# Kernel tuning notes

Hardware: AMD Instinct MI355X
Metric: run time of the kernel (lower is better)

Reference implementation:

```python
import jax, jax.numpy as jnp
import numpy as np

KNN_K = 8
WINDOW = 3  # temporal_window + 1 candidate frames
LN_EPS = 1e-5
NORM_EPS = 1e-12


def setup_inputs() -> dict:
    key = jax.random.key(0)
    B, T, M, D, H = 2, 8, 512, 1024, 1024
    ks = jax.random.split(key, 12)
    s = 0.02
    return {
        "z": jax.random.normal(ks[0], (B, T, M, D), jnp.float32),
        "Wq": jax.random.normal(ks[1], (D, D), jnp.float32) * s,
        "Wv": jax.random.normal(ks[2], (D, D), jnp.float32) * s,
        "Wout": jax.random.normal(ks[3], (D, D), jnp.float32) * s,
        "ln_w": jnp.ones((D,), jnp.float32),
        "ln_b": jnp.zeros((D,), jnp.float32),
        "Watt_q": jax.random.normal(ks[4], (D, D), jnp.float32) * s,
        "Watt_k": jax.random.normal(ks[5], (D, D), jnp.float32) * s,
        "W_ih": jax.random.normal(ks[6], (3 * H, D), jnp.float32) * s,
        "W_hh": jax.random.normal(ks[7], (3 * H, H), jnp.float32) * s,
        "b_ih": jnp.zeros((3 * H,), jnp.float32),
        "b_hh": jnp.zeros((3 * H,), jnp.float32),
        "W_mf": jax.random.normal(ks[8], (D, H), jnp.float32) * s,
        "b_mf": jnp.zeros((D,), jnp.float32),
    }


def _forward(z, Wq, Wv, Wout, ln_w, ln_b, Watt_q, Watt_k,
             W_ih, W_hh, b_ih, b_hh, W_mf, b_mf):
    B, T, M, D = z.shape
    H = W_hh.shape[1]
    # cosine normalization (torch F.normalize with eps clamp)
    zn = z / jnp.maximum(jnp.linalg.norm(z, axis=-1, keepdims=True), NORM_EPS)
    mem = jnp.zeros((B, M, H), z.dtype)
    b_ar = jnp.arange(B)[:, None, None]
    outs = []
    for t in range(T):  # T is static; fully vectorized over B, M, k inside
        tts = t - jnp.arange(WINDOW)          # candidate frames t, t-1, t-2
        valid = tts >= 0                      # [W]
        cand = zn[:, jnp.clip(tts, 0)]        # [B,W,M,D]
        # cosine similarity query nodes at t vs all candidates (dt-major order)
        sim = jnp.einsum('bmd,bwnd->bmwn', zn[:, t], cand).reshape(B, M, WINDOW * M)
        sim = jnp.where(jnp.repeat(valid, M)[None, None, :], sim, -jnp.inf)
        vals, idx = jax.lax.top_k(sim, KNN_K)  # [B,M,k]
        dt = idx // M
        j = idx % M
        tt = jnp.clip(t - dt, 0)
        Kfeat = z[b_ar, tt, j]                 # [B,M,k,D] gathered neighbors
        # GAT quirk faithful to source: scalar logit scale from node 0's query,
        # first output coordinate only, shared across all nodes of (b,t)
        s0 = z[:, t, 0] @ Watt_q[0]            # [B]
        kh_sum = (Kfeat @ Watt_k.T).sum(-1)    # [B,M,k]
        att = jax.nn.softmax(s0[:, None, None] * kh_sum, axis=-1)
        alpha = 0.5 * vals + 0.5 * att         # [B,M,k]
        msg = jnp.einsum('bmk,bmkd->bmd', alpha, Kfeat @ Wv.T)
        h_t = z[:, t]                          # [B,M,D]
        x = msg + h_t @ Wq.T
        mu = x.mean(-1, keepdims=True)
        var = ((x - mu) ** 2).mean(-1, keepdims=True)
        x = (x - mu) / jnp.sqrt(var + LN_EPS) * ln_w + ln_b
        inp = x @ Wout.T
        # torch GRUCell: gates ordered (r, z, n)
        gi = inp @ W_ih.T + b_ih               # [B,M,3H]
        gh = mem @ W_hh.T + b_hh
        ir, iz, inn = jnp.split(gi, 3, axis=-1)
        hr, hz, hn = jnp.split(gh, 3, axis=-1)
        r = jax.nn.sigmoid(ir + hr)
        zg = jax.nn.sigmoid(iz + hz)
        n = jnp.tanh(inn + r * hn)
        mem = (1.0 - zg) * n + zg * mem
        outs.append(h_t + mem @ W_mf.T + b_mf)
    h = jnp.stack(outs, axis=1)                # [B,T,M,D]
    return h, mem


def reference(z, Wq, Wv, Wout, ln_w, ln_b, Watt_q, Watt_k,
              W_ih, W_hh, b_ih, b_hh, W_mf, b_mf):
    return _forward(z, Wq, Wv, Wout, ln_w, ln_b, Watt_q, Watt_k,
                    W_ih, W_hh, b_ih, b_hh, W_mf, b_mf)
```

## Files before the change

### kernel.cpp

```cpp
#include <hip/hip_runtime.h>
#include <hip/hip_bf16.h>
#include <math.h>

#define B_ 2
#define T_ 8
#define M_ 512
#define D_ 1024
#define H_ 1024
#define NC_ 1536
#define KNN 8

typedef __hip_bfloat16 bf16;
typedef short v8s __attribute__((ext_vector_type(8)));
typedef float v4f __attribute__((ext_vector_type(4)));

__device__ __forceinline__ float b2f(short s) {
  union { unsigned u; float f; } x; x.u = ((unsigned)(unsigned short)s) << 16; return x.f;
}

__device__ __forceinline__ void async16(const void* g, void* l) {
  __builtin_amdgcn_global_load_lds(
      (const __attribute__((address_space(1))) void*)g,
      (__attribute__((address_space(3))) void*)l, 16, 0, 0);
}

__device__ __forceinline__ void mfma_loop(const bf16* __restrict__ A,
                                          const bf16* __restrict__ Bp,
                                          int K, v4f (&acc)[4][4],
                                          bf16* sA, bf16* sB)
{
  const int tid  = threadIdx.x;
  const int lane = tid & 63;
  const int wave = tid >> 6;
  const int quad = lane >> 4;
  const int l15  = lane & 15;
  const int wr = (wave >> 1) * 64;
  const int wc = (wave & 1) * 64;

  const int r0 = tid >> 2, g0 = (tid & 3) ^ ((r0 >> 1) & 3);
  const int c1 = tid + 256;
  const int r1 = c1 >> 2,  g1 = (c1 & 3) ^ ((r1 >> 1) & 3);

  const bf16* a0p = A  + (size_t)r0*K + g0*8;
  const bf16* a1p = A  + (size_t)r1*K + g1*8;
  const bf16* b0p = Bp + (size_t)r0*K + g0*8;
  const bf16* b1p = Bp + (size_t)r1*K + g1*8;
  bf16* la0 = sA + tid*8;  bf16* la1 = sA + c1*8;
  bf16* lb0 = sB + tid*8;  bf16* lb1 = sB + c1*8;

  int aoff[4], boff[4];
  #pragma unroll
  for (int i = 0; i < 4; ++i) {
    int ra = wr + i*16 + l15;
    aoff[i] = (ra*4 + (quad ^ ((ra >> 1) & 3))) * 8;
    int rb = wc + i*16 + l15;
    boff[i] = (rb*4 + (quad ^ ((rb >> 1) & 3))) * 8;
  }

  for (int k0 = 0; k0 < K; k0 += 32) {
    __syncthreads();
    async16(a0p + k0, la0);
    async16(a1p + k0, la1);
    async16(b0p + k0, lb0);
    async16(b1p + k0, lb1);
    __syncthreads();
    v8s af[4], bfr[4];
    #pragma unroll
    for (int i = 0; i < 4; ++i) af[i]  = *(const v8s*)(sA + aoff[i]);
    #pragma unroll
    for (int i = 0; i < 4; ++i) bfr[i] = *(const v8s*)(sB + boff[i]);
    #pragma unroll
    for (int mi = 0; mi < 4; ++mi)
      #pragma unroll
      for (int ni = 0; ni < 4; ++ni)
        acc[mi][ni] = __builtin_amdgcn_mfma_f32_16x16x32_bf16(
            af[mi], bfr[ni], acc[mi][ni], 0, 0, 0);
  }
}

template<bool DUAL, bool HASBIAS, bool HASADD, bool OUTBF>
__global__ __launch_bounds__(256) void k_bgemm(
    const bf16* __restrict__ A1, const bf16* __restrict__ B1,
    const bf16* __restrict__ A2, const bf16* __restrict__ B2,
    const float* __restrict__ bias, const float* __restrict__ add,
    void* __restrict__ Cv, int N, int K)
{
  __shared__ bf16 sA[128*32];
  __shared__ bf16 sB[128*32];
  v4f acc[4][4];
  #pragma unroll
  for (int i = 0; i < 4; ++i)
    #pragma unroll
    for (int j = 0; j < 4; ++j) acc[i][j] = (v4f){0.f,0.f,0.f,0.f};

  const int row0 = blockIdx.y * 128, col0 = blockIdx.x * 128;
  mfma_loop(A1 + (size_t)row0*K, B1 + (size_t)col0*K, K, acc, sA, sB);
  if constexpr (DUAL)
    mfma_loop(A2 + (size_t)row0*K, B2 + (size_t)col0*K, K, acc, sA, sB);

  const int tid = threadIdx.x, lane = tid & 63, wave = tid >> 6;
  const int quad = lane >> 4, l15 = lane & 15;
  const int wr = (wave >> 1) * 64, wc = (wave & 1) * 64;

  #pragma unroll
  for (int ni = 0; ni < 4; ++ni) {
    const int col = col0 + wc + ni*16 + l15;
    float bv = 0.f;
    if constexpr (HASBIAS) bv = bias[col];
    #pragma unroll
    for (int mi = 0; mi < 4; ++mi) {
      const int rowb = row0 + wr + mi*16 + quad*4;
      #pragma unroll
      for (int reg = 0; reg < 4; ++reg) {
        const int row = rowb + reg;
        float v = acc[mi][ni][reg] + bv;
        if constexpr (HASADD) v += add[(size_t)row*N + col];
        if constexpr (OUTBF)
          ((bf16*)Cv)[(size_t)row*N + col] = __float2bfloat16(v);
        else
          ((float*)Cv)[(size_t)row*N + col] = v;
      }
    }
  }
}

__global__ __launch_bounds__(256) void k_sims(const bf16* __restrict__ znhi,
                                              const bf16* __restrict__ znlo,
                                              float* __restrict__ sim)
{
  __shared__ bf16 sAh[128*32];
  __shared__ bf16 sAl[128*32];
  __shared__ bf16 sBh[128*32];
  __shared__ bf16 sBl[128*32];

  const int zi = blockIdx.z;
  const int w  = zi % 3;
  const int bt = zi / 3;
  const int b  = bt / T_;
  const int t  = bt % T_;
  if (w > t) return;
  const int tw = t - w;
  const int arow0 = bt*M_ + blockIdx.y*128;
  const int brow0 = (b*T_ + tw)*M_ + blockIdx.x*128;

  const bf16* Ah = znhi + (size_t)arow0*D_;
  const bf16* Al = znlo + (size_t)arow0*D_;
  const bf16* Bh = znhi + (size_t)brow0*D_;
  const bf16* Bl = znlo + (size_t)brow0*D_;

  v4f acc[4][4];
  #pragma unroll
  for (int i = 0; i < 4; ++i)
    #pragma unroll
    for (int j = 0; j < 4; ++j) acc[i][j] = (v4f){0.f,0.f,0.f,0.f};

  const int tid  = threadIdx.x;
  const int lane = tid & 63;
  const int wave = tid >> 6;
  const int quad = lane >> 4;
  const int l15  = lane & 15;
  const int wr = (wave >> 1) * 64;
  const int wc = (wave & 1) * 64;

  const int r0 = tid >> 2, g0 = (tid & 3) ^ ((r0 >> 1) & 3);
  const int c1 = tid + 256;
  const int r1 = c1 >> 2,  g1 = (c1 & 3) ^ ((r1 >> 1) & 3);
  const size_t o0 = (size_t)r0*D_ + g0*8;
  const size_t o1 = (size_t)r1*D_ + g1*8;

  int aoff[4], boff[4];
  #pragma unroll
  for (int i = 0; i < 4; ++i) {
    int ra = wr + i*16 + l15;
    aoff[i] = (ra*4 + (quad ^ ((ra >> 1) & 3))) * 8;
    int rb = wc + i*16 + l15;
    boff[i] = (rb*4 + (quad ^ ((rb >> 1) & 3))) * 8;
  }

  for (int k0 = 0; k0 < D_; k0 += 32) {
    __syncthreads();
    async16(Ah + o0 + k0, sAh + tid*8);
    async16(Ah + o1 + k0, sAh + c1*8);
    async16(Al + o0 + k0, sAl + tid*8);
    async16(Al + o1 + k0, sAl + c1*8);
    async16(Bh + o0 + k0, sBh + tid*8);
    async16(Bh + o1 + k0, sBh + c1*8);
    async16(Bl + o0 + k0, sBl + tid*8);
    async16(Bl + o1 + k0, sBl + c1*8);
    __syncthreads();
    v8s ah[4], al[4], bh[4], bl[4];
    #pragma unroll
    for (int i = 0; i < 4; ++i) {
      ah[i] = *(const v8s*)(sAh + aoff[i]);
      al[i] = *(const v8s*)(sAl + aoff[i]);
      bh[i] = *(const v8s*)(sBh + boff[i]);
      bl[i] = *(const v8s*)(sBl + boff[i]);
    }
    #pragma unroll
    for (int mi = 0; mi < 4; ++mi)
      #pragma unroll
      for (int ni = 0; ni < 4; ++ni) {
        acc[mi][ni] = __builtin_amdgcn_mfma_f32_16x16x32_bf16(ah[mi], bh[ni], acc[mi][ni], 0, 0, 0);
        acc[mi][ni] = __builtin_amdgcn_mfma_f32_16x16x32_bf16(ah[mi], bl[ni], acc[mi][ni], 0, 0, 0);
        acc[mi][ni] = __builtin_amdgcn_mfma_f32_16x16x32_bf16(al[mi], bh[ni], acc[mi][ni], 0, 0, 0);
      }
  }

  float* C = sim + (size_t)bt*M_*NC_;
  const int rowbase = blockIdx.y*128 + wr;
  const int colbase = w*M_ + blockIdx.x*128 + wc;
  #pragma unroll
  for (int ni = 0; ni < 4; ++ni) {
    const int col = colbase + ni*16 + l15;
    #pragma unroll
    for (int mi = 0; mi < 4; ++mi) {
      const int rowb = rowbase + mi*16 + quad*4;
      #pragma unroll
      for (int reg = 0; reg < 4; ++reg)
        C[(size_t)(rowb+reg)*NC_ + col] = acc[mi][ni][reg];
    }
  }
}


__global__ __launch_bounds__(256) void k_cast(const float* __restrict__ src,
                                              bf16* __restrict__ dst, int n4) {
  int i = blockIdx.x*256 + threadIdx.x;
  if (i < n4) {
    float4 v = ((const float4*)src)[i];
    bf16* p = dst + (size_t)i*4;
    p[0] = __float2bfloat16(v.x); p[1] = __float2bfloat16(v.y);
    p[2] = __float2bfloat16(v.z); p[3] = __float2bfloat16(v.w);
  }
}

__global__ __launch_bounds__(256) void k_colsum(const float* __restrict__ Wk,
                                                float* __restrict__ wk_sum) {
  int d = blockIdx.x*256 + threadIdx.x;
  float s = 0.f;
  for (int i = 0; i < D_; ++i) s += Wk[(size_t)i*D_ + d];
  wk_sum[d] = s;
}

__global__ __launch_bounds__(64) void k_s0(const float* __restrict__ z,
                                           const float* __restrict__ Wattq,
                                           float* __restrict__ s0) {
  int bt = blockIdx.x;
  const float* zr = z + (size_t)bt*M_*D_;
  float p = 0.f;
  for (int d = threadIdx.x; d < D_; d += 64) p += zr[d]*Wattq[d];
  for (int o = 32; o; o >>= 1) p += __shfl_down(p, o, 64);
  if (threadIdx.x == 0) s0[bt] = p;
}

__global__ __launch_bounds__(256) void k_kh(const float* __restrict__ z,
                                            const float* __restrict__ wks,
                                            float* __restrict__ kh) {
  int wave = threadIdx.x >> 6, l = threadIdx.x & 63;
  int r = blockIdx.x*4 + wave;
  const float* zp = z + (size_t)r*D_ + l*16;
  const float* wp = wks + l*16;
  float p = 0.f;
  #pragma unroll
  for (int j = 0; j < 4; ++j) {
    float4 a = *(const float4*)(zp + j*4);
    float4 b = *(const float4*)(wp + j*4);
    p += a.x*b.x + a.y*b.y + a.z*b.z + a.w*b.w;
  }
  for (int o = 32; o; o >>= 1) p += __shfl_down(p, o, 64);
  if (l == 0) kh[r] = p;
}

__global__ __launch_bounds__(256) void k_znsplit(const float* __restrict__ z,
                                                 bf16* __restrict__ znhi,
                                                 bf16* __restrict__ znlo) {
  int row = blockIdx.x, tid = threadIdx.x;
  const float* zr = z + (size_t)row*D_;
  int d = tid*4;
  float4 v = *(const float4*)(zr + d);
  float ss = v.x*v.x + v.y*v.y + v.z*v.z + v.w*v.w;
  for (int o=32;o;o>>=1) ss += __shfl_down(ss,o,64);
  __shared__ float ps[4];
  if ((tid&63)==0) ps[tid>>6] = ss;
  __syncthreads();
  float s = ps[0]+ps[1]+ps[2]+ps[3];
  float rn = 1.0f / fmaxf(sqrtf(s), 1e-12f);
  float zn[4] = {v.x*rn, v.y*rn, v.z*rn, v.w*rn};
  bf16 hi[4], lo[4];
  #pragma unroll
  for (int j = 0; j < 4; ++j) {
    hi[j] = __float2bfloat16(zn[j]);
    lo[j] = __float2bfloat16(zn[j] - b2f(*(short*)&hi[j]));
  }
  *(short4*)(znhi + (size_t)row*D_ + d) = *(short4*)hi;
  *(short4*)(znlo + (size_t)row*D_ + d) = *(short4*)lo;
}

__global__ __launch_bounds__(256) void k_topk(
    const float* __restrict__ sim, const float* __restrict__ kh,
    const float* __restrict__ s0, const bf16* __restrict__ zb,
    bf16* __restrict__ kbarb)
{
  const int wave = threadIdx.x >> 6, l = threadIdx.x & 63;
  const int r  = blockIdx.x*4 + wave;
  const int bt = r >> 9, m = r & 511;
  const int b  = bt >> 3, t = bt & 7;
  const float* srow = sim + (size_t)bt*M_*NC_ + (size_t)m*NC_;
  const int limit = (t >= 2) ? NC_ : ((t == 1) ? 2*M_ : M_);

  float v[24];
  #pragma unroll
  for (int j = 0; j < 24; ++j) {
    int i = j*64 + l;
    v[j] = (i < limit) ? srow[i] : -INFINITY;
  }

  float selv[KNN]; int seli[KNN];
  #pragma unroll
  for (int k = 0; k < KNN; ++k) {
    float bv = v[0]; int bj = 0;
    #pragma unroll
    for (int j = 1; j < 24; ++j)
      if (v[j] > bv) { bv = v[j]; bj = j; }
    int bi = bj*64 + l;
    #pragma unroll
    for (int o = 1; o < 64; o <<= 1) {
      float ov = __shfl_xor(bv, o, 64);
      int   oi = __shfl_xor(bi, o, 64);
      if (ov > bv || (ov == bv && oi < bi)) { bv = ov; bi = oi; }
    }
    selv[k] = bv; seli[k] = bi;
    if ((bi & 63) == l) {
      int jj = bi >> 6;
      #pragma unroll
      for (int j = 0; j < 24; ++j) if (j == jj) v[j] = -INFINITY;
    }
  }

  float khv = 0.f;
  if (l < KNN) {
    int idx = seli[l];
    int w = idx >> 9, n = idx & 511;
    int tt = t - w;
    khv = kh[(b*T_ + tt)*M_ + n];
  }
  float s0v = s0[bt];
  float att[KNN], mx = -INFINITY;
  #pragma unroll
  for (int k = 0; k < KNN; ++k) { att[k] = s0v * __shfl(khv, k, 64); mx = fmaxf(mx, att[k]); }
  float den = 0.f;
  #pragma unroll
  for (int k = 0; k < KNN; ++k) { att[k] = expf(att[k]-mx); den += att[k]; }
  float rden = 1.0f/den;
  float alpha[KNN];
  #pragma unroll
  for (int k = 0; k < KNN; ++k) alpha[k] = 0.5f*selv[k] + 0.5f*att[k]*rden;

  const int d0 = l*16;
  float o[16];
  #pragma unroll
  for (int e = 0; e < 16; ++e) o[e] = 0.f;
  #pragma unroll
  for (int k = 0; k < KNN; ++k) {
    int idx = seli[k];
    int w = idx >> 9, n = idx & 511;
    int tt = t - w;
    const bf16* zp = zb + ((size_t)((b*T_ + tt)*M_ + n))*D_ + d0;
    v8s z0 = *(const v8s*)zp;
    v8s z1 = *(const v8s*)(zp + 8);
    float al = alpha[k];
    #pragma unroll
    for (int e = 0; e < 8; ++e) {
      o[e]   = fmaf(al, b2f(z0[e]), o[e]);
      o[8+e] = fmaf(al, b2f(z1[e]), o[8+e]);
    }
  }
  bf16* kp = kbarb + (size_t)r*D_ + d0;
  short outv[16];
  #pragma unroll
  for (int e = 0; e < 16; ++e) { bf16 h = __float2bfloat16(o[e]); outv[e] = *(short*)&h; }
  *(v8s*)kp       = *(v8s*)outv;
  *(v8s*)(kp + 8) = *(v8s*)(outv + 8);
}

__global__ __launch_bounds__(256) void k_ln(const float* __restrict__ X,
                                            const float* __restrict__ lw,
                                            const float* __restrict__ lb,
                                            bf16* __restrict__ Xb) {
  int r = blockIdx.x, tid = threadIdx.x;
  const float* xp = X + (size_t)r*D_;
  int d = tid*4;
  float4 v = *(const float4*)(xp + d);
  float s  = v.x+v.y+v.z+v.w;
  float ss = v.x*v.x+v.y*v.y+v.z*v.z+v.w*v.w;
  for (int o=32;o;o>>=1){ s += __shfl_down(s,o,64); ss += __shfl_down(ss,o,64); }
  __shared__ float rs[4], rss[4];
  if ((tid&63)==0){ rs[tid>>6]=s; rss[tid>>6]=ss; }
  __syncthreads();
  float mu  = (rs[0]+rs[1]+rs[2]+rs[3]) * (1.f/D_);
  float var = (rss[0]+rss[1]+rss[2]+rss[3]) * (1.f/D_) - mu*mu;
  float rstd = rsqrtf(var + 1e-5f);
  float4 w  = *(const float4*)(lw+d);
  float4 bb = *(const float4*)(lb+d);
  bf16* op = Xb + (size_t)r*D_ + d;
  op[0] = __float2bfloat16((v.x-mu)*rstd*w.x + bb.x);
  op[1] = __float2bfloat16((v.y-mu)*rstd*w.y + bb.y);
  op[2] = __float2bfloat16((v.z-mu)*rstd*w.z + bb.z);
  op[3] = __float2bfloat16((v.w-mu)*rstd*w.w + bb.w);
}

__global__ __launch_bounds__(256) void k_gru(
    const float* __restrict__ gi, const float* __restrict__ gh,
    float* __restrict__ mem, bf16* __restrict__ memb,
    bf16* __restrict__ memhb, int t)
{
  int gid = blockIdx.x*256 + threadIdx.x;
  int row = gid >> 10, h = gid & 1023;
  int b = row >> 9, m = row & 511;
  size_t girow = ((size_t)((b*T_ + t)*M_ + m))*(3*H_);
  float ir  = gi[girow + h];
  float iz  = gi[girow + H_ + h];
  float in_ = gi[girow + 2*H_ + h];
  size_t ghrow = (size_t)row*(3*H_);
  float hr = gh[ghrow + h];
  float hz = gh[ghrow + H_ + h];
  float hn = gh[ghrow + 2*H_ + h];
  float rg = 1.f/(1.f+expf(-(ir+hr)));
  float zg = 1.f/(1.f+expf(-(iz+hz)));
  float n  = tanhf(in_ + rg*hn);
  float mold = mem[gid];
  float mnew = (1.f-zg)*n + zg*mold;
  mem[gid] = mnew;
  memb[gid] = __float2bfloat16(mnew);
  memhb[((size_t)((b*T_ + t)*M_ + m))*H_ + h] = __float2bfloat16(mnew);
}

extern "C" void kernel_launch(void* const* d_in, const int* in_sizes, int n_in,
                              void* d_out, int out_size, void* d_ws, size_t ws_size,
                              hipStream_t stream) {
  (void)in_sizes; (void)n_in; (void)out_size; (void)ws_size;
  const float* z      = (const float*)d_in[0];
  const float* Wq     = (const float*)d_in[1];
  const float* Wv     = (const float*)d_in[2];
  const float* Wout   = (const float*)d_in[3];
  const float* ln_w   = (const float*)d_in[4];
  const float* ln_b   = (const float*)d_in[5];
  const float* Watt_q = (const float*)d_in[6];
  const float* Watt_k = (const float*)d_in[7];
  const float* W_ih   = (const float*)d_in[8];
  const float* W_hh   = (const float*)d_in[9];
  const float* b_ih   = (const float*)d_in[10];
  const float* b_hh   = (const float*)d_in[11];
  const float* W_mf   = (const float*)d_in[12];
  const float* b_mf   = (const float*)d_in[13];
  float* out = (float*)d_out;
  float* ws  = (float*)d_ws;

  float* GI    = ws;
  float* sim   = ws;
  float* X     = ws;
  float* gs    = ws + 25165824;
  float* mem   = ws + 28311552;
  bf16*  Xb    = (bf16*)(ws + 29360128);
  bf16*  znhi  = Xb;
  bf16*  zb    = (bf16*)(ws + 33554432);
  bf16*  kbarb = (bf16*)(ws + 37748736);
  bf16*  INPb  = kbarb;
  bf16*  memb  = (bf16*)(ws + 41943040);
  bf16*  memhb = (bf16*)(ws + 42467328);
  bf16*  znlo  = memhb;
  bf16*  Wqb   = (bf16*)(ws + 46661632);
  bf16*  Wvb   = Wqb + 1048576;
  bf16*  Woutb = Wqb + 2097152;
  bf16*  Wihb  = Wqb + 3145728;
  bf16*  Whhb  = Wqb + 6291456;
  bf16*  Wmfb  = Wqb + 9437184;
  float* wks   = ws + 51904512;
  float* s0    = ws + 51905536;
  float* kh    = ws + 51905552;

  k_cast<<<dim3(1024), dim3(256), 0, stream>>>(Wq,   Wqb,   262144);
  k_cast<<<dim3(1024), dim3(256), 0, stream>>>(Wv,   Wvb,   262144);
  k_cast<<<dim3(1024), dim3(256), 0, stream>>>(Wout, Woutb, 262144);
  k_cast<<<dim3(3072), dim3(256), 0, stream>>>(W_ih, Wihb,  786432);
  k_cast<<<dim3(3072), dim3(256), 0, stream>>>(W_hh, Whhb,  786432);
  k_cast<<<dim3(1024), dim3(256), 0, stream>>>(W_mf, Wmfb,  262144);
  k_cast<<<dim3(8192), dim3(256), 0, stream>>>(z,    zb,   2097152);

  k_colsum <<<dim3(4),    dim3(256), 0, stream>>>(Watt_k, wks);
  k_s0     <<<dim3(16),   dim3(64),  0, stream>>>(z, Watt_q, s0);
  k_kh     <<<dim3(2048), dim3(256), 0, stream>>>(z, wks, kh);
  k_znsplit<<<dim3(8192), dim3(256), 0, stream>>>(z, znhi, znlo);

  k_sims<<<dim3(4,4,48), dim3(256), 0, stream>>>(znhi, znlo, sim);

  k_topk<<<dim3(2048), dim3(256), 0, stream>>>(sim, kh, s0, zb, kbarb);

  k_bgemm<true,false,false,false><<<dim3(8,64), dim3(256), 0, stream>>>(
      kbarb, Wvb, zb, Wqb, nullptr, nullptr, X, D_, D_);

  k_ln<<<dim3(8192), dim3(256), 0, stream>>>(X, ln_w, ln_b, Xb);

  k_bgemm<false,false,false,true><<<dim3(8,64), dim3(256), 0, stream>>>(
      Xb, Woutb, nullptr, nullptr, nullptr, nullptr, INPb, D_, D_);

  k_bgemm<false,true,false,false><<<dim3(24,64), dim3(256), 0, stream>>>(
      INPb, Wihb, nullptr, nullptr, b_ih, nullptr, GI, 3*H_, D_);

  hipMemsetAsync(mem,  0, (size_t)1048576*sizeof(float), stream);
  hipMemsetAsync(memb, 0, (size_t)1048576*sizeof(bf16),  stream);

  for (int t = 0; t < T_; ++t) {
    k_bgemm<false,true,false,false><<<dim3(24,8), dim3(256), 0, stream>>>(
        memb, Whhb, nullptr, nullptr, b_hh, nullptr, gs, 3*H_, H_);
    k_gru<<<dim3(4096), dim3(256), 0, stream>>>(GI, gs, mem, memb, memhb, t);
  }

  k_bgemm<false,true,true,false><<<dim3(8,64), dim3(256), 0, stream>>>(
      memhb, Wmfb, nullptr, nullptr, b_mf, z, out, D_, H_);

  hipMemcpyAsync(out + (size_t)B_*T_*M_*D_, mem, (size_t)1048576*sizeof(float),
                 hipMemcpyDeviceToDevice, stream);
}
```

Before: 827.0 us.

## Fuse GRU gate GEMM with cell update, merge prep kernels, store bf16 intermediates

Replaces the per-step W_hh GEMM plus separate GRU elementwise kernel with one fused kernel that computes all three gate tiles in registers and applies the GRU update in the epilogue. The hidden-state bf16 buffer is ping-ponged between steps to avoid read/write races. The six weight casts become one launch, the z cast, norm split and kh dot product are merged into one pass over z, and the X and GI intermediates are stored as bf16 instead of fp32. Together these cut launches and memory traffic, but the bf16 X and GI add rounding error, and the fused GRU grid is small (128 blocks) with no k-loop pipelining.

New measurement: 858.7 us. 1.04x slower.

```diff
diff --git a/kernel.cpp b/kernel.cpp
--- a/kernel.cpp
+++ b/kernel.cpp
@@ -16,6 +16,9 @@
 
 __device__ __forceinline__ float b2f(short s) {
   union { unsigned u; float f; } x; x.u = ((unsigned)(unsigned short)s) << 16; return x.f;
+}
+__device__ __forceinline__ short f2b(float f) {
+  bf16 h = __float2bfloat16(f); return *(short*)&h;
 }
 
 __device__ __forceinline__ void async16(const void* g, void* l) {
@@ -222,16 +225,135 @@
   }
 }
 
-
-__global__ __launch_bounds__(256) void k_cast(const float* __restrict__ src,
-                                              bf16* __restrict__ dst, int n4) {
+__global__ __launch_bounds__(256) void k_fgru(
+    const bf16* __restrict__ membIn, const bf16* __restrict__ Whhb,
+    const bf16* __restrict__ gib, const float* __restrict__ b_hh,
+    float* __restrict__ mem, bf16* __restrict__ membOut,
+    bf16* __restrict__ memhb, int t)
+{
+  __shared__ bf16 sA[128*32];
+  __shared__ bf16 sB[3][64*32];
+
+  const int row0 = blockIdx.y * 128;
+  const int col0 = blockIdx.x * 64;
+
+  v4f acc[3][4][2];
+  #pragma unroll
+  for (int g = 0; g < 3; ++g)
+    #pragma unroll
+    for (int i = 0; i < 4; ++i)
+      #pragma unroll
+      for (int j = 0; j < 2; ++j) acc[g][i][j] = (v4f){0.f,0.f,0.f,0.f};
+
+  const int tid  = threadIdx.x;
+  const int lane = tid & 63;
+  const int wave = tid >> 6;
+  const int quad = lane >> 4;
+  const int l15  = lane & 15;
+  const int wr = (wave >> 1) * 64;
+  const int wc = (wave & 1) * 32;
+
+  const int rA0 = tid >> 2, gA0 = (tid & 3) ^ ((rA0 >> 1) & 3);
+  const int c1 = tid + 256;
+  const int rA1 = c1 >> 2,  gA1 = (c1 & 3) ^ ((rA1 >> 1) & 3);
+  const int rB = tid >> 2,  gB  = (tid & 3) ^ ((rB >> 1) & 3);
+
+  const bf16* Ap = membIn + (size_t)row0*H_;
+  const size_t aofs0 = (size_t)rA0*H_ + gA0*8;
+  const size_t aofs1 = (size_t)rA1*H_ + gA1*8;
+  const size_t bofs  = (size_t)(col0 + rB)*H_ + gB*8;
+
+  int aoff[4], boff[2];
+  #pragma unroll
+  for (int i = 0; i < 4; ++i) {
+    int ra = wr + i*16 + l15;
+    aoff[i] = (ra*4 + (quad ^ ((ra >> 1) & 3))) * 8;
+  }
+  #pragma unroll
+  for (int i = 0; i < 2; ++i) {
+    int rb = wc + i*16 + l15;
+    boff[i] = (rb*4 + (quad ^ ((rb >> 1) & 3))) * 8;
+  }
+
+  for (int k0 = 0; k0 < H_; k0 += 32) {
+    __syncthreads();
+    async16(Ap + aofs0 + k0, sA + tid*8);
+    async16(Ap + aofs1 + k0, sA + c1*8);
+    async16(Whhb + bofs + k0,           sB[0] + tid*8);
+    async16(Whhb + 1048576 + bofs + k0, sB[1] + tid*8);
+    async16(Whhb + 2097152 + bofs + k0, sB[2] + tid*8);
+    __syncthreads();
+    v8s af[4], bfr[3][2];
+    #pragma unroll
+    for (int i = 0; i < 4; ++i) af[i] = *(const v8s*)(sA + aoff[i]);
+    #pragma unroll
+    for (int g = 0; g < 3; ++g)
+      #pragma unroll
+      for (int i = 0; i < 2; ++i) bfr[g][i] = *(const v8s*)(sB[g] + boff[i]);
+    #pragma unroll
+    for (int g = 0; g < 3; ++g)
+      #pragma unroll
+      for (int mi = 0; mi < 4; ++mi)
+        #pragma unroll
+        for (int ni = 0; ni < 2; ++ni)
+          acc[g][mi][ni] = __builtin_amdgcn_mfma_f32_16x16x32_bf16(
+              af[mi], bfr[g][ni], acc[g][mi][ni], 0, 0, 0);
+  }
+
+  #pragma unroll
+  for (int ni = 0; ni < 2; ++ni) {
+    const int col = col0 + wc + ni*16 + l15;
+    const float bhr = b_hh[col];
+    const float bhz = b_hh[H_ + col];
+    const float bhn = b_hh[2*H_ + col];
+    #pragma unroll
+    for (int mi = 0; mi < 4; ++mi) {
+      const int rowb = row0 + wr + mi*16 + quad*4;
+      #pragma unroll
+      for (int reg = 0; reg < 4; ++reg) {
+        const int row = rowb + reg;
+        const int b = row >> 9, m = row & 511;
+        const size_t btm = (size_t)((b*T_ + t)*M_ + m);
+        const bf16* gp = gib + btm*(3*H_);
+        float ir  = b2f(*(const short*)(gp + col));
+        float iz  = b2f(*(const short*)(gp + H_ + col));
+        float inn = b2f(*(const short*)(gp + 2*H_ + col));
+        float hr = acc[0][mi][ni][reg] + bhr;
+        float hz = acc[1][mi][ni][reg] + bhz;
+        float hn = acc[2][mi][ni][reg] + bhn;
+        float rg = 1.f/(1.f + expf(-(ir + hr)));
+        float zg = 1.f/(1.f + expf(-(iz + hz)));
+        float n  = tanhf(inn + rg*hn);
+        const size_t mo = (size_t)row*H_ + col;
+        float mold = mem[mo];
+        float mnew = (1.f - zg)*n + zg*mold;
+        mem[mo] = mnew;
+        bf16 mb = __float2bfloat16(mnew);
+        membOut[mo] = mb;
+        memhb[btm*H_ + col] = mb;
+      }
+    }
+  }
+}
+
+
+__global__ __launch_bounds__(256) void k_castall(
+    const float* __restrict__ w0, const float* __restrict__ w1,
+    const float* __restrict__ w2, const float* __restrict__ w3,
+    const float* __restrict__ w4, const float* __restrict__ w5,
+    bf16* __restrict__ dst)
+{
   int i = blockIdx.x*256 + threadIdx.x;
-  if (i < n4) {
-    float4 v = ((const float4*)src)[i];
-    bf16* p = dst + (size_t)i*4;
-    p[0] = __float2bfloat16(v.x); p[1] = __float2bfloat16(v.y);
-    p[2] = __float2bfloat16(v.z); p[3] = __float2bfloat16(v.w);
-  }
+  const float* src; int base;
+  if      (i <  262144) { src = w0; base = 0; }
+  else if (i <  524288) { src = w1; base = 262144; }
+  else if (i <  786432) { src = w2; base = 524288; }
+  else if (i < 1572864) { src = w3; base = 786432; }
+  else if (i < 2359296) { src = w4; base = 1572864; }
+  else                  { src = w5; base = 2359296; }
+  float4 v = ((const float4*)src)[i - base];
+  short4 o = make_short4(f2b(v.x), f2b(v.y), f2b(v.z), f2b(v.w));
+  *(short4*)(dst + (size_t)i*4) = o;
 }
 
 __global__ __launch_bounds__(256) void k_colsum(const float* __restrict__ Wk,
@@ -253,31 +375,17 @@
   if (threadIdx.x == 0) s0[bt] = p;
 }
 
-__global__ __launch_bounds__(256) void k_kh(const float* __restrict__ z,
-                                            const float* __restrict__ wks,
-                                            float* __restrict__ kh) {
-  int wave = threadIdx.x >> 6, l = threadIdx.x & 63;
-  int r = blockIdx.x*4 + wave;
-  const float* zp = z + (size_t)r*D_ + l*16;
-  const float* wp = wks + l*16;
-  float p = 0.f;
-  #pragma unroll
-  for (int j = 0; j < 4; ++j) {
-    float4 a = *(const float4*)(zp + j*4);
-    float4 b = *(const float4*)(wp + j*4);
-    p += a.x*b.x + a.y*b.y + a.z*b.z + a.w*b.w;
-  }
-  for (int o = 32; o; o >>= 1) p += __shfl_down(p, o, 64);
-  if (l == 0) kh[r] = p;
-}
-
-__global__ __launch_bounds__(256) void k_znsplit(const float* __restrict__ z,
-                                                 bf16* __restrict__ znhi,
-                                                 bf16* __restrict__ znlo) {
+__global__ __launch_bounds__(256) void k_zprep(const float* __restrict__ z,
+                                               const float* __restrict__ wks,
+                                               bf16* __restrict__ zb,
+                                               bf16* __restrict__ znhi,
+                                               bf16* __restrict__ znlo,
+                                               float* __restrict__ kh) {
   int row = blockIdx.x, tid = threadIdx.x;
   const float* zr = z + (size_t)row*D_;
   int d = tid*4;
   float4 v = *(const float4*)(zr + d);
+
   float ss = v.x*v.x + v.y*v.y + v.z*v.z + v.w*v.w;
   for (int o=32;o;o>>=1) ss += __shfl_down(ss,o,64);
   __shared__ float ps[4];
@@ -285,15 +393,26 @@
   __syncthreads();
   float s = ps[0]+ps[1]+ps[2]+ps[3];
   float rn = 1.0f / fmaxf(sqrtf(s), 1e-12f);
+
+  *(short4*)(zb + (size_t)row*D_ + d) = make_short4(f2b(v.x), f2b(v.y), f2b(v.z), f2b(v.w));
+
   float zn[4] = {v.x*rn, v.y*rn, v.z*rn, v.w*rn};
-  bf16 hi[4], lo[4];
+  short hi[4], lo[4];
   #pragma unroll
   for (int j = 0; j < 4; ++j) {
-    hi[j] = __float2bfloat16(zn[j]);
-    lo[j] = __float2bfloat16(zn[j] - b2f(*(short*)&hi[j]));
-  }
-  *(short4*)(znhi + (size_t)row*D_ + d) = *(short4*)hi;
-  *(short4*)(znlo + (size_t)row*D_ + d) = *(short4*)lo;
+    hi[j] = f2b(zn[j]);
+    lo[j] = f2b(zn[j] - b2f(hi[j]));
+  }
+  *(short4*)(znhi + (size_t)row*D_ + d) = make_short4(hi[0],hi[1],hi[2],hi[3]);
+  *(short4*)(znlo + (size_t)row*D_ + d) = make_short4(lo[0],lo[1],lo[2],lo[3]);
+
+  float4 w = *(const float4*)(wks + d);
+  float p = v.x*w.x + v.y*w.y + v.z*w.z + v.w*w.w;
+  for (int o=32;o;o>>=1) p += __shfl_down(p,o,64);
+  __shared__ float pk[4];
+  if ((tid&63)==0) pk[tid>>6] = p;
+  __syncthreads();
+  if (tid==0) kh[row] = pk[0]+pk[1]+pk[2]+pk[3];
 }
 
 __global__ __launch_bounds__(256) void k_topk(
@@ -378,21 +497,21 @@
   bf16* kp = kbarb + (size_t)r*D_ + d0;
   short outv[16];
   #pragma unroll
-  for (int e = 0; e < 16; ++e) { bf16 h = __float2bfloat16(o[e]); outv[e] = *(short*)&h; }
+  for (int e = 0; e < 16; ++e) outv[e] = f2b(o[e]);
   *(v8s*)kp       = *(v8s*)outv;
   *(v8s*)(kp + 8) = *(v8s*)(outv + 8);
 }
 
-__global__ __launch_bounds__(256) void k_ln(const float* __restrict__ X,
+__global__ __launch_bounds__(256) void k_ln(const bf16* __restrict__ X,
                                             const float* __restrict__ lw,
                                             const float* __restrict__ lb,
                                             bf16* __restrict__ Xb) {
   int r = blockIdx.x, tid = threadIdx.x;
-  const float* xp = X + (size_t)r*D_;
   int d = tid*4;
-  float4 v = *(const float4*)(xp + d);
-  float s  = v.x+v.y+v.z+v.w;
-  float ss = v.x*v.x+v.y*v.y+v.z*v.z+v.w*v.w;
+  short4 sv = *(const short4*)(X + (size_t)r*D_ + d);
+  float v0 = b2f(sv.x), v1 = b2f(sv.y), v2 = b2f(sv.z), v3 = b2f(sv.w);
+  float s  = v0+v1+v2+v3;
+  float ss = v0*v0+v1*v1+v2*v2+v3*v3;
   for (int o=32;o;o>>=1){ s += __shfl_down(s,o,64); ss += __shfl_down(ss,o,64); }
   __shared__ float rs[4], rss[4];
   if ((tid&63)==0){ rs[tid>>6]=s; rss[tid>>6]=ss; }
@@ -402,37 +521,10 @@
   float rstd = rsqrtf(var + 1e-5f);
   float4 w  = *(const float4*)(lw+d);
   float4 bb = *(const float4*)(lb+d);
-  bf16* op = Xb + (size_t)r*D_ + d;
-  op[0] = __float2bfloat16((v.x-mu)*rstd*w.x + bb.x);
-  op[1] = __float2bfloat16((v.y-mu)*rstd*w.y + bb.y);
-  op[2] = __float2bfloat16((v.z-mu)*rstd*w.z + bb.z);
-  op[3] = __float2bfloat16((v.w-mu)*rstd*w.w + bb.w);
-}
-
-__global__ __launch_bounds__(256) void k_gru(
-    const float* __restrict__ gi, const float* __restrict__ gh,
-    float* __restrict__ mem, bf16* __restrict__ memb,
-    bf16* __restrict__ memhb, int t)
-{
-  int gid = blockIdx.x*256 + threadIdx.x;
-  int row = gid >> 10, h = gid & 1023;
-  int b = row >> 9, m = row & 511;
-  size_t girow = ((size_t)((b*T_ + t)*M_ + m))*(3*H_);
-  float ir  = gi[girow + h];
-  float iz  = gi[girow + H_ + h];
-  float in_ = gi[girow + 2*H_ + h];
-  size_t ghrow = (size_t)row*(3*H_);
-  float hr = gh[ghrow + h];
-  float hz = gh[ghrow + H_ + h];
-  float hn = gh[ghrow + 2*H_ + h];
-  float rg = 1.f/(1.f+expf(-(ir+hr)));
-  float zg = 1.f/(1.f+expf(-(iz+hz)));
-  float n  = tanhf(in_ + rg*hn);
-  float mold = mem[gid];
-  float mnew = (1.f-zg)*n + zg*mold;
-  mem[gid] = mnew;
-  memb[gid] = __float2bfloat16(mnew);
-  memhb[((size_t)((b*T_ + t)*M_ + m))*H_ + h] = __float2bfloat16(mnew);
+  short4 o = make_short4(
+      f2b((v0-mu)*rstd*w.x + bb.x), f2b((v1-mu)*rstd*w.y + bb.y),
+      f2b((v2-mu)*rstd*w.z + bb.z), f2b((v3-mu)*rstd*w.w + bb.w));
+  *(short4*)(Xb + (size_t)r*D_ + d) = o;
 }
 
 extern "C" void kernel_launch(void* const* d_in, const int* in_sizes, int n_in,
@@ -456,64 +548,57 @@
   float* out = (float*)d_out;
   float* ws  = (float*)d_ws;
 
-  float* GI    = ws;
   float* sim   = ws;
-  float* X     = ws;
-  float* gs    = ws + 25165824;
-  float* mem   = ws + 28311552;
-  bf16*  Xb    = (bf16*)(ws + 29360128);
-  bf16*  znhi  = Xb;
-  bf16*  zb    = (bf16*)(ws + 33554432);
-  bf16*  kbarb = (bf16*)(ws + 37748736);
+  bf16*  XB0   = (bf16*)ws;
+  bf16*  GIb   = (bf16*)ws;
+  float* mem   = ws + 12582912;
+  bf16*  membA = (bf16*)(ws + 13631488);
+  bf16*  membB = (bf16*)(ws + 14155776);
+  bf16*  znhi  = (bf16*)(ws + 14680064);
+  bf16*  Xb    = znhi;
+  bf16*  zb    = (bf16*)(ws + 18874368);
+  bf16*  kbarb = (bf16*)(ws + 23068672);
   bf16*  INPb  = kbarb;
-  bf16*  memb  = (bf16*)(ws + 41943040);
-  bf16*  memhb = (bf16*)(ws + 42467328);
+  bf16*  memhb = (bf16*)(ws + 27262976);
   bf16*  znlo  = memhb;
-  bf16*  Wqb   = (bf16*)(ws + 46661632);
+  bf16*  Wqb   = (bf16*)(ws + 31457280);
   bf16*  Wvb   = Wqb + 1048576;
   bf16*  Woutb = Wqb + 2097152;
   bf16*  Wihb  = Wqb + 3145728;
   bf16*  Whhb  = Wqb + 6291456;
   bf16*  Wmfb  = Wqb + 9437184;
-  float* wks   = ws + 51904512;
-  float* s0    = ws + 51905536;
-  float* kh    = ws + 51905552;
-
-  k_cast<<<dim3(1024), dim3(256), 0, stream>>>(Wq,   Wqb,   262144);
-  k_cast<<<dim3(1024), dim3(256), 0, stream>>>(Wv,   Wvb,   262144);
-  k_cast<<<dim3(1024), dim3(256), 0, stream>>>(Wout, Woutb, 262144);
-  k_cast<<<dim3(3072), dim3(256), 0, stream>>>(W_ih, Wihb,  786432);
-  k_cast<<<dim3(3072), dim3(256), 0, stream>>>(W_hh, Whhb,  786432);
-  k_cast<<<dim3(1024), dim3(256), 0, stream>>>(W_mf, Wmfb,  262144);
-  k_cast<<<dim3(8192), dim3(256), 0, stream>>>(z,    zb,   2097152);
-
-  k_colsum <<<dim3(4),    dim3(256), 0, stream>>>(Watt_k, wks);
-  k_s0     <<<dim3(16),   dim3(64),  0, stream>>>(z, Watt_q, s0);
-  k_kh     <<<dim3(2048), dim3(256), 0, stream>>>(z, wks, kh);
-  k_znsplit<<<dim3(8192), dim3(256), 0, stream>>>(z, znhi, znlo);
+  float* wks   = ws + 36700160;
+  float* s0    = ws + 36701184;
+  float* kh    = ws + 36701200;
+
+  k_castall<<<dim3(10240), dim3(256), 0, stream>>>(Wq, Wv, Wout, W_ih, W_hh, W_mf, Wqb);
+  k_colsum <<<dim3(4),     dim3(256), 0, stream>>>(Watt_k, wks);
+  k_s0     <<<dim3(16),    dim3(64),  0, stream>>>(z, Watt_q, s0);
+  k_zprep  <<<dim3(8192),  dim3(256), 0, stream>>>(z, wks, zb, znhi, znlo, kh);
 
   k_sims<<<dim3(4,4,48), dim3(256), 0, stream>>>(znhi, znlo, sim);
 
   k_topk<<<dim3(2048), dim3(256), 0, stream>>>(sim, kh, s0, zb, kbarb);
 
-  k_bgemm<true,false,false,false><<<dim3(8,64), dim3(256), 0, stream>>>(
-      kbarb, Wvb, zb, Wqb, nullptr, nullptr, X, D_, D_);
-
-  k_ln<<<dim3(8192), dim3(256), 0, stream>>>(X, ln_w, ln_b, Xb);
+  k_bgemm<true,false,false,true><<<dim3(8,64), dim3(256), 0, stream>>>(
+      kbarb, Wvb, zb, Wqb, nullptr, nullptr, XB0, D_, D_);
+
+  k_ln<<<dim3(8192), dim3(256), 0, stream>>>(XB0, ln_w, ln_b, Xb);
 
   k_bgemm<false,false,false,true><<<dim3(8,64), dim3(256), 0, stream>>>(
       Xb, Woutb, nullptr, nullptr, nullptr, nullptr, INPb, D_, D_);
 
-  k_bgemm<false,true,false,false><<<dim3(24,64), dim3(256), 0, stream>>>(
-      INPb, Wihb, nullptr, nullptr, b_ih, nullptr, GI, 3*H_, D_);
-
-  hipMemsetAsync(mem,  0, (size_t)1048576*sizeof(float), stream);
-  hipMemsetAsync(memb, 0, (size_t)1048576*sizeof(bf16),  stream);
+  k_bgemm<false,true,false,true><<<dim3(24,64), dim3(256), 0, stream>>>(
+      INPb, Wihb, nullptr, nullptr, b_ih, nullptr, GIb, 3*H_, D_);
+
+  hipMemsetAsync(mem,   0, (size_t)1048576*sizeof(float), stream);
+  hipMemsetAsync(membA, 0, (size_t)1048576*sizeof(bf16),  stream);
 
   for (int t = 0; t < T_; ++t) {
-    k_bgemm<false,true,false,false><<<dim3(24,8), dim3(256), 0, stream>>>(
-        memb, Whhb, nullptr, nullptr, b_hh, nullptr, gs, 3*H_, H_);
-    k_gru<<<dim3(4096), dim3(256), 0, stream>>>(GI, gs, mem, memb, memhb, t);
+    const bf16* min_ = (t & 1) ? membB : membA;
+    bf16*       mout = (t & 1) ? membA : membB;
+    k_fgru<<<dim3(16,8), dim3(256), 0, stream>>>(
+        min_, Whhb, GIb, b_hh, mem, mout, memhb, t);
   }
 
   k_bgemm<false,true,true,false><<<dim3(8,64), dim3(256), 0, stream>>>(
```
